# Kernel optimization log

Measured on AMD Instinct MI355X. Metric: run time of the kernel, lower is better.

The kernel has to match this reference:

```python
import jax, jax.numpy as jnp
import numpy as np

L, H, C, V, T_BLK = 12, 12, 768, 50257, 1024
D = C // H  # head dim = 64


def _layernorm(x, g, b, eps=1e-5):
    m = jnp.mean(x, axis=-1, keepdims=True)
    v = jnp.mean(jnp.square(x - m), axis=-1, keepdims=True)
    return (x - m) * jax.lax.rsqrt(v + eps) * g + b


def setup_inputs() -> dict:
    key = jax.random.key(0)
    ks = jax.random.split(key, 8)
    B, T = 8, 1024
    s = 0.02
    sp = 0.02 / np.sqrt(2 * L)  # c_proj special init
    return {
        "idx": jax.random.randint(ks[0], (B, T), 0, V, dtype=jnp.int32),
        "wte": jax.random.normal(ks[1], (V, C), jnp.float32) * s,
        "wpe": jax.random.normal(ks[2], (T_BLK, C), jnp.float32) * s,
        "ln1_g": jnp.ones((L, C), jnp.float32),
        "ln1_b": jnp.zeros((L, C), jnp.float32),
        "w_qkv": jax.random.normal(ks[3], (L, C, 3 * C), jnp.float32) * s,
        "b_qkv": jnp.zeros((L, 3 * C), jnp.float32),
        "w_ao": jax.random.normal(ks[4], (L, C, C), jnp.float32) * sp,
        "b_ao": jnp.zeros((L, C), jnp.float32),
        "ln2_g": jnp.ones((L, C), jnp.float32),
        "ln2_b": jnp.zeros((L, C), jnp.float32),
        "w_fc": jax.random.normal(ks[5], (L, C, 4 * C), jnp.float32) * s,
        "b_fc": jnp.zeros((L, 4 * C), jnp.float32),
        "w_mo": jax.random.normal(ks[6], (L, 4 * C, C), jnp.float32) * sp,
        "b_mo": jnp.zeros((L, C), jnp.float32),
        "lnf_g": jnp.ones((C,), jnp.float32),
        "lnf_b": jnp.zeros((C,), jnp.float32),
    }


def reference(idx, wte, wpe, ln1_g, ln1_b, w_qkv, b_qkv, w_ao, b_ao,
              ln2_g, ln2_b, w_fc, b_fc, w_mo, b_mo, lnf_g, lnf_b):
    B, T = idx.shape
    scale = 1.0 / np.sqrt(D)
    causal = jnp.tril(jnp.ones((T, T), dtype=bool))  # [T,T]

    x = wte[idx] + wpe[:T]  # [B,T,C]

    def block(x, p):
        g1, b1, wq, bq, wo, bo, g2, b2_, wf, bf, w2, b2m = p
        h = _layernorm(x, g1, b1)
        qkv = h @ wq + bq  # [B,T,3C]
        q, k, v = jnp.split(qkv, 3, axis=-1)
        q = q.reshape(B, T, H, D)
        k = k.reshape(B, T, H, D)
        v = v.reshape(B, T, H, D)
        att = jnp.einsum('bqhd,bkhd->bhqk', q, k) * scale
        att = jnp.where(causal, att, -jnp.inf)
        att = jax.nn.softmax(att, axis=-1)
        y = jnp.einsum('bhqk,bkhd->bqhd', att, v).reshape(B, T, C)
        x = x + y @ wo + bo
        h2 = _layernorm(x, g2, b2_)
        x = x + jax.nn.gelu(h2 @ wf + bf, approximate=False) @ w2 + b2m
        return x, None

    params = (ln1_g, ln1_b, w_qkv, b_qkv, w_ao, b_ao,
              ln2_g, ln2_b, w_fc, b_fc, w_mo, b_mo)
    x, _ = jax.lax.scan(block, x, params)

    x = _layernorm(x, lnf_g, lnf_b)
    # inference path: logits only for last position, lm_head tied to wte
    logits = x[:, -1:, :] @ wte.T  # [B,1,V]
    return logits
```

## Files before the change

### kernel.cpp

```cpp
#include <hip/hip_runtime.h>

#define B_ 8
#define T_ 1024
#define C_ 768
#define H_ 12
#define L_ 12
#define V_ 50257

typedef __bf16 bf16_t;
typedef __bf16 bf16x8 __attribute__((ext_vector_type(8)));
typedef __bf16 bf16x4 __attribute__((ext_vector_type(4)));
typedef float f32x4 __attribute__((ext_vector_type(4)));

#define AS1 __attribute__((address_space(1)))
#define AS3 __attribute__((address_space(3)))

__device__ __forceinline__ unsigned short f2bf(float f) {
  bf16_t h = (bf16_t)f;
  return __builtin_bit_cast(unsigned short, h);
}

__device__ __forceinline__ unsigned short bfbits(bf16_t h) {
  return __builtin_bit_cast(unsigned short, h);
}

__device__ __forceinline__ float fast_gelu(float v) {
  const float xe = v * 0.70710678118f;
  const float ax = fabsf(xe);
  const float t = 1.0f / fmaf(0.3275911f, ax, 1.0f);
  float poly = fmaf(t, 1.061405429f, -1.453152027f);
  poly = fmaf(t, poly, 1.421413741f);
  poly = fmaf(t, poly, -0.284496736f);
  poly = fmaf(t, poly, 0.254829592f);
  poly *= t;
  float er = 1.0f - poly * __expf(-ax * ax);
  er = (xe < 0.0f) ? -er : er;
  return 0.5f * v * (1.0f + er);
}

template<int CTRL>
__device__ __forceinline__ float dppf(float x) {
  return __builtin_bit_cast(float, __builtin_amdgcn_update_dpp(
      0, __builtin_bit_cast(int, x), CTRL, 0xF, 0xF, true));
}
__device__ __forceinline__ float red16_max(float x) {
  x = fmaxf(x, dppf<0xB1>(x));
  x = fmaxf(x, dppf<0x4E>(x));
  x = fmaxf(x, dppf<0x124>(x));
  x = fmaxf(x, dppf<0x128>(x));
  return x;
}
__device__ __forceinline__ float red16_sum(float x) {
  x += dppf<0xB1>(x);
  x += dppf<0x4E>(x);
  x += dppf<0x124>(x);
  x += dppf<0x128>(x);
  return x;
}

__global__ __launch_bounds__(192) void embed_kernel(
    const int* __restrict__ idx, const float* __restrict__ wte,
    const float* __restrict__ wpe, float* __restrict__ xf)
{
  const int bt = blockIdx.x;
  const int t = bt & (T_ - 1);
  const int tok = idx[bt];
  const int c4 = threadIdx.x << 2;
  float4 a = *(const float4*)(wte + (size_t)tok * C_ + c4);
  float4 p = *(const float4*)(wpe + (size_t)t * C_ + c4);
  float4 r; r.x = a.x + p.x; r.y = a.y + p.y; r.z = a.z + p.z; r.w = a.w + p.w;
  *(float4*)(xf + (size_t)bt * C_ + c4) = r;
}

template<bool LAST>
__global__ __launch_bounds__(256) void ln_kernel(
    const float* __restrict__ x, const float* __restrict__ gw,
    const float* __restrict__ bw, unsigned short* __restrict__ obf,
    float* __restrict__ of)
{
  __shared__ float red[8];
  const size_t row = LAST ? ((size_t)blockIdx.x * T_ + (T_ - 1)) : (size_t)blockIdx.x;
  const float* xr = x + row * C_;
  const int t = threadIdx.x;
  float v0 = xr[t], v1 = xr[t + 256], v2 = xr[t + 512];
  float s = v0 + v1 + v2;
  #pragma unroll
  for (int off = 32; off; off >>= 1) s += __shfl_xor(s, off);
  if ((t & 63) == 0) red[t >> 6] = s;
  __syncthreads();
  const float mean = (red[0] + red[1] + red[2] + red[3]) * (1.0f / C_);
  const float d0 = v0 - mean, d1 = v1 - mean, d2 = v2 - mean;
  float ss = d0 * d0 + d1 * d1 + d2 * d2;
  #pragma unroll
  for (int off = 32; off; off >>= 1) ss += __shfl_xor(ss, off);
  if ((t & 63) == 0) red[4 + (t >> 6)] = ss;
  __syncthreads();
  const float var = (red[4] + red[5] + red[6] + red[7]) * (1.0f / C_);
  const float rs = rsqrtf(var + 1e-5f);
  float o0 = d0 * rs * gw[t] + bw[t];
  float o1 = d1 * rs * gw[t + 256] + bw[t + 256];
  float o2 = d2 * rs * gw[t + 512] + bw[t + 512];
  if (LAST) {
    float* orow = of + (size_t)blockIdx.x * C_;
    orow[t] = o0; orow[t + 256] = o1; orow[t + 512] = o2;
  } else {
    unsigned short* orow = obf + row * C_;
    orow[t] = f2bf(o0); orow[t + 256] = f2bf(o1); orow[t + 512] = f2bf(o2);
  }
}

__global__ __launch_bounds__(256) void cvtw4_kernel(
    const float* __restrict__ wq, const float* __restrict__ wa,
    const float* __restrict__ wf, const float* __restrict__ wm,
    unsigned short* __restrict__ out)
{
  __shared__ float tile[32][33];
  const int i = blockIdx.x;
  const float* W; unsigned short* Wt; int K, N, tix;
  if (i < 1728)      { W = wq; Wt = out;                 K = C_;     N = 3 * C_; tix = i; }
  else if (i < 2304) { W = wa; Wt = out + 3 * C_ * C_;   K = C_;     N = C_;     tix = i - 1728; }
  else if (i < 4608) { W = wf; Wt = out + 4 * C_ * C_;   K = C_;     N = 4 * C_; tix = i - 2304; }
  else               { W = wm; Wt = out + 8 * C_ * C_;   K = 4 * C_; N = C_;     tix = i - 4608; }
  const int ntx = N >> 5;
  const int kb = (tix / ntx) << 5, nb = (tix % ntx) << 5;
  const int t = threadIdx.x;
  {
    const int k = t >> 3, n4 = (t & 7) << 2;
    float4 v = *(const float4*)(W + (size_t)(kb + k) * N + nb + n4);
    tile[k][n4] = v.x; tile[k][n4 + 1] = v.y; tile[k][n4 + 2] = v.z; tile[k][n4 + 3] = v.w;
  }
  __syncthreads();
  {
    const int n = t >> 3, k4 = (t & 7) << 2;
    ushort4 o;
    o.x = f2bf(tile[k4][n]);     o.y = f2bf(tile[k4 + 1][n]);
    o.z = f2bf(tile[k4 + 2][n]); o.w = f2bf(tile[k4 + 3][n]);
    *(ushort4*)(Wt + (size_t)(nb + n) * K + kb + k4) = o;
  }
}

template<int EPI>
__global__ __launch_bounds__(256, 2) void gemm_bt(
    const unsigned short* __restrict__ A, const unsigned short* __restrict__ Bt,
    const float* __restrict__ bias, float* __restrict__ Cf,
    unsigned short* __restrict__ Cb, int M, int N, int K, int nx)
{
  (void)M; (void)nx;
  __shared__ unsigned short As[2][128 * 64];
  __shared__ unsigned short Bs[2][128 * 64];
  const int tid = threadIdx.x;
  const int lane = tid & 63;
  const int w = tid >> 6;
  const int wr = w >> 1, wc = w & 1;
  const int l15 = lane & 15, l4 = lane >> 4;
  const int swz = lane & 7;

  const int bid = blockIdx.x;
  const int xcd = bid & 7;
  const int j = bid >> 3;
  const int mblk = xcd * 8 + (j & 7);
  const int nblk = j >> 3;
  const int m0 = mblk * 128, n0 = nblk * 128;

  f32x4 acc[4][4] = {};

  const int srow = lane >> 3;
  const int schunk = (lane & 7) ^ srow;
  const unsigned short* aSrc = A + (size_t)(m0 + w * 32 + srow) * K + schunk * 8;
  const unsigned short* bSrc = Bt + (size_t)(n0 + w * 32 + srow) * K + schunk * 8;
  const int ldsRowBase = (w * 32) * 64;

  auto stage = [&](int kt, int p) {
    const int k0 = kt << 6;
    #pragma unroll
    for (int jj = 0; jj < 4; ++jj)
      __builtin_amdgcn_global_load_lds(
          (const AS1 unsigned int*)(aSrc + (size_t)jj * 8 * K + k0),
          (AS3 unsigned int*)(&As[p][ldsRowBase + jj * 8 * 64]), 16, 0, 0);
    #pragma unroll
    for (int jj = 0; jj < 4; ++jj)
      __builtin_amdgcn_global_load_lds(
          (const AS1 unsigned int*)(bSrc + (size_t)jj * 8 * K + k0),
          (AS3 unsigned int*)(&Bs[p][ldsRowBase + jj * 8 * 64]), 16, 0, 0);
  };

  auto compute = [&](int p) {
    const unsigned short* aw = &As[p][(wr * 64) * 64];
    const unsigned short* bw2 = &Bs[p][(wc * 64) * 64];
    #pragma unroll
    for (int ks = 0; ks < 2; ++ks) {
      bf16x8 af[4], bf[4];
      #pragma unroll
      for (int mf = 0; mf < 4; ++mf)
        af[mf] = *(const bf16x8*)(aw + (mf * 16 + l15) * 64 + (((ks << 2) | l4) ^ swz) * 8);
      #pragma unroll
      for (int nf = 0; nf < 4; ++nf)
        bf[nf] = *(const bf16x8*)(bw2 + (nf * 16 + l15) * 64 + (((ks << 2) | l4) ^ swz) * 8);
      __builtin_amdgcn_s_setprio(1);
      #pragma unroll
      for (int mf = 0; mf < 4; ++mf)
        #pragma unroll
        for (int nf = 0; nf < 4; ++nf)
          acc[mf][nf] = __builtin_amdgcn_mfma_f32_16x16x32_bf16(af[mf], bf[nf], acc[mf][nf], 0, 0, 0);
      __builtin_amdgcn_s_setprio(0);
    }
  };

  const int nk = K >> 6;
  stage(0, 0);
  for (int kt = 0; kt < nk - 1; ++kt) {
    const int p = kt & 1;
    stage(kt + 1, p ^ 1);
    asm volatile("s_waitcnt vmcnt(8)" ::: "memory");
    __builtin_amdgcn_s_barrier();
    compute(p);
    __builtin_amdgcn_s_barrier();
  }
  asm volatile("s_waitcnt vmcnt(0)" ::: "memory");
  __builtin_amdgcn_s_barrier();
  compute((nk - 1) & 1);

  #pragma unroll
  for (int mf = 0; mf < 4; ++mf) {
    #pragma unroll
    for (int nf = 0; nf < 4; ++nf) {
      const int col = n0 + wc * 64 + nf * 16 + l15;
      const float bv = bias[col];
      int hh = 0, dd = 0;
      unsigned short* qkvo = nullptr;
      if constexpr (EPI == 3) {
        const int which = col / C_;
        const int rem = col - which * C_;
        hh = rem >> 6; dd = rem & 63;
        qkvo = Cb + (size_t)which * ((size_t)B_ * H_ * T_ * 64);
      }
      #pragma unroll
      for (int i = 0; i < 4; ++i) {
        const int row = m0 + wr * 64 + mf * 16 + l4 * 4 + i;
        float v = acc[mf][nf][i] + bv;
        if constexpr (EPI == 1) {
          Cf[(size_t)row * N + col] += v;
        } else if constexpr (EPI == 2) {
          Cb[(size_t)row * N + col] = f2bf(fast_gelu(v));
        } else {
          const int bb = row >> 10, tt = row & (T_ - 1);
          qkvo[(((size_t)bb * H_ + hh) * T_ + tt) * 64 + dd] = f2bf(v);
        }
      }
    }
  }
}

__global__ __launch_bounds__(256) void attn_kernel(
    const unsigned short* __restrict__ Qb, const unsigned short* __restrict__ Kb,
    const unsigned short* __restrict__ Vb, unsigned short* __restrict__ y)
{
  const int pb = blockIdx.x / 96;
  const int bh = blockIdx.x % 96;
  const int h = bh % H_;
  const int b = bh / H_;
  const int tid = threadIdx.x, lane = tid & 63, w = tid >> 6;
  const int l15 = lane & 15, l4 = lane >> 4;

  const int qband0 = pb * 64 + w * 16;
  const int qband1 = (15 - pb) * 64 + w * 16;
  const int NT = (17 - pb) >> 1;

  __shared__ unsigned short Ks[128 * 64];
  __shared__ unsigned short Vt[64 * 136];
  __shared__ unsigned short Pb[4][32 * 74];

  bf16x8 qf[2][2];
  {
    const unsigned short* q0p = Qb + ((size_t)bh * T_ + qband0) * 64;
    const unsigned short* q1p = Qb + ((size_t)bh * T_ + qband1) * 64;
    #pragma unroll
    for (int ks = 0; ks < 2; ++ks) {
      qf[0][ks] = *(const bf16x8*)(q0p + l15 * 64 + ks * 32 + l4 * 8);
      qf[1][ks] = *(const bf16x8*)(q1p + l15 * 64 + ks * 32 + l4 * 8);
    }
  }

  f32x4 o[2][4] = {};
  float mrow[2][4], lrow[2][4];
  #pragma unroll
  for (int mf = 0; mf < 2; ++mf)
    #pragma unroll
    for (int i = 0; i < 4; ++i) { mrow[mf][i] = -1e30f; lrow[mf][i] = 0.0f; }

  const unsigned short* kb0 = Kb + (size_t)bh * T_ * 64;
  const unsigned short* vb0 = Vb + (size_t)bh * T_ * 64;
  const int ck = w;
  const int skey = lane;
  const int sw = (skey & 7);

  bf16x8 kr0, kr1, kr2, kr3, vr0, vr1, vr2, vr3;
  {
    const unsigned short* kp = kb0 + (size_t)skey * 64;
    const unsigned short* vp = vb0 + (size_t)skey * 64;
    kr0 = *(const bf16x8*)(kp + ck * 8);
    kr1 = *(const bf16x8*)(kp + (ck + 4) * 8);
    kr2 = *(const bf16x8*)(kp + 64 * 64 + ck * 8);
    kr3 = *(const bf16x8*)(kp + 64 * 64 + (ck + 4) * 8);
    vr0 = *(const bf16x8*)(vp + ck * 8);
    vr1 = *(const bf16x8*)(vp + (ck + 4) * 8);
    vr2 = *(const bf16x8*)(vp + 64 * 64 + ck * 8);
    vr3 = *(const bf16x8*)(vp + 64 * 64 + (ck + 4) * 8);
  }

  for (int kt = 0; kt < NT; ++kt) {
    const int k0 = kt << 7;
    __syncthreads();
    *(bf16x8*)(Ks + skey * 64 + ((ck ^ sw) * 8)) = kr0;
    *(bf16x8*)(Ks + skey * 64 + (((ck + 4) ^ sw) * 8)) = kr1;
    *(bf16x8*)(Ks + (skey + 64) * 64 + ((ck ^ sw) * 8)) = kr2;
    *(bf16x8*)(Ks + (skey + 64) * 64 + (((ck + 4) ^ sw) * 8)) = kr3;
    #pragma unroll
    for (int jj = 0; jj < 8; ++jj) {
      Vt[(ck * 8 + jj) * 136 + skey]            = bfbits(vr0[jj]);
      Vt[((ck + 4) * 8 + jj) * 136 + skey]      = bfbits(vr1[jj]);
      Vt[(ck * 8 + jj) * 136 + skey + 64]       = bfbits(vr2[jj]);
      Vt[((ck + 4) * 8 + jj) * 136 + skey + 64] = bfbits(vr3[jj]);
    }
    __syncthreads();
    if (kt + 1 < NT) {
      const int kn = (kt + 1) << 7;
      const unsigned short* kp = kb0 + (size_t)(kn + skey) * 64;
      const unsigned short* vp = vb0 + (size_t)(kn + skey) * 64;
      kr0 = *(const bf16x8*)(kp + ck * 8);
      kr1 = *(const bf16x8*)(kp + (ck + 4) * 8);
      kr2 = *(const bf16x8*)(kp + 64 * 64 + ck * 8);
      kr3 = *(const bf16x8*)(kp + 64 * 64 + (ck + 4) * 8);
      vr0 = *(const bf16x8*)(vp + ck * 8);
      vr1 = *(const bf16x8*)(vp + (ck + 4) * 8);
      vr2 = *(const bf16x8*)(vp + 64 * 64 + ck * 8);
      vr3 = *(const bf16x8*)(vp + 64 * 64 + (ck + 4) * 8);
    }

    #pragma unroll
    for (int h2 = 0; h2 < 2; ++h2) {
      const int kh0 = k0 + h2 * 64;
      const bool act0 = (kh0 <= qband0 + 15);
      const bool act1 = (kh0 <= qband1 + 15);
      if (!act0 && !act1) continue;

      f32x4 s[2][4] = {};
      __builtin_amdgcn_s_setprio(1);
      #pragma unroll
      for (int ks = 0; ks < 2; ++ks) {
        #pragma unroll
        for (int nfk = 0; nfk < 4; ++nfk) {
          const int key = h2 * 64 + nfk * 16 + l15;
          bf16x8 kf = *(const bf16x8*)(Ks + key * 64 + ((((ks << 2) | l4) ^ (l15 & 7)) * 8));
          if (act0) s[0][nfk] = __builtin_amdgcn_mfma_f32_16x16x32_bf16(qf[0][ks], kf, s[0][nfk], 0, 0, 0);
          if (act1) s[1][nfk] = __builtin_amdgcn_mfma_f32_16x16x32_bf16(qf[1][ks], kf, s[1][nfk], 0, 0, 0);
        }
      }
      __builtin_amdgcn_s_setprio(0);

      #pragma unroll
      for (int mf = 0; mf < 2; ++mf) {
        const bool act = mf ? act1 : act0;
        if (!act) continue;
        const int qb0 = mf ? qband1 : qband0;
        const int qrow = qb0 + l4 * 4;
        const bool fullt = (kh0 + 63) <= qb0;
        float pvv[4][4], tm[4];
        #pragma unroll
        for (int i = 0; i < 4; ++i) {
          const int q = qrow + i;
          float m_ = -1e30f;
          #pragma unroll
          for (int nfk = 0; nfk < 4; ++nfk) {
            float x = s[mf][nfk][i] * 0.125f;
            x = fullt ? x : ((kh0 + nfk * 16 + l15 <= q) ? x : -1e30f);
            pvv[nfk][i] = x;
            m_ = fmaxf(m_, x);
          }
          tm[i] = red16_max(m_);
        }
        bool need = false;
        #pragma unroll
        for (int i = 0; i < 4; ++i) need |= (tm[i] > mrow[mf][i] + 8.0f);
        if (__any(need)) {
          #pragma unroll
          for (int i = 0; i < 4; ++i) {
            const float mnew = fmaxf(mrow[mf][i], tm[i]);
            const float alpha = __expf(mrow[mf][i] - mnew);
            mrow[mf][i] = mnew;
            lrow[mf][i] *= alpha;
            #pragma unroll
            for (int nf = 0; nf < 4; ++nf) o[mf][nf][i] *= alpha;
          }
        }
        #pragma unroll
        for (int i = 0; i < 4; ++i) {
          float rsum = 0.0f;
          #pragma unroll
          for (int nfk = 0; nfk < 4; ++nfk) {
            const float p = __expf(pvv[nfk][i] - mrow[mf][i]);
            pvv[nfk][i] = p; rsum += p;
          }
          rsum = red16_sum(rsum);
          lrow[mf][i] += rsum;
        }
        #pragma unroll
        for (int nfk = 0; nfk < 4; ++nfk)
          #pragma unroll
          for (int i = 0; i < 4; ++i)
            Pb[w][(mf * 16 + l4 * 4 + i) * 74 + nfk * 16 + l15] = f2bf(pvv[nfk][i]);
      }

      bf16x8 pa[2][2];
      #pragma unroll
      for (int mf = 0; mf < 2; ++mf)
        if (mf ? act1 : act0)
          #pragma unroll
          for (int k2 = 0; k2 < 2; ++k2)
            pa[mf][k2] = *(const bf16x8*)(Pb[w] + (mf * 16 + l15) * 74 + k2 * 32 + l4 * 8);
      __builtin_amdgcn_s_setprio(1);
      #pragma unroll
      for (int nf = 0; nf < 4; ++nf) {
        const int d = nf * 16 + l15;
        #pragma unroll
        for (int k2 = 0; k2 < 2; ++k2) {
          bf16x8 vf = *(const bf16x8*)(Vt + d * 136 + h2 * 64 + k2 * 32 + l4 * 8);
          if (act0) o[0][nf] = __builtin_amdgcn_mfma_f32_16x16x32_bf16(pa[0][k2], vf, o[0][nf], 0, 0, 0);
          if (act1) o[1][nf] = __builtin_amdgcn_mfma_f32_16x16x32_bf16(pa[1][k2], vf, o[1][nf], 0, 0, 0);
        }
      }
      __builtin_amdgcn_s_setprio(0);
    }
  }

  #pragma unroll
  for (int mf = 0; mf < 2; ++mf) {
    const int qb0 = mf ? qband1 : qband0;
    #pragma unroll
    for (int i = 0; i < 4; ++i) {
      const float inv = 1.0f / lrow[mf][i];
      const int q = qb0 + l4 * 4 + i;
      unsigned short* yr = y + (size_t)(b * T_ + q) * C_ + h * 64;
      #pragma unroll
      for (int nf = 0; nf < 4; ++nf)
        yr[nf * 16 + l15] = f2bf(o[mf][nf][i] * inv);
    }
  }
}

__global__ __launch_bounds__(256) void head_kernel(
    const float* __restrict__ lnf, const float* __restrict__ wte,
    float* __restrict__ out)
{
  __shared__ float xs[B_ * C_];
  for (int i = threadIdx.x; i < B_ * C_; i += 256) xs[i] = lnf[i];
  __syncthreads();
  const int w = threadIdx.x >> 6, lane = threadIdx.x & 63;
  const int v = blockIdx.x * 4 + w;
  if (v >= V_) return;
  const float* wv = wte + (size_t)v * C_ + lane * 12;
  float4 w0 = *(const float4*)(wv);
  float4 w1 = *(const float4*)(wv + 4);
  float4 w2 = *(const float4*)(wv + 8);
  float acc[B_];
  #pragma unroll
  for (int bb = 0; bb < B_; ++bb) {
    const float* xr = xs + bb * C_ + lane * 12;
    float4 x0 = *(const float4*)(xr);
    float4 x1 = *(const float4*)(xr + 4);
    float4 x2 = *(const float4*)(xr + 8);
    acc[bb] = w0.x * x0.x + w0.y * x0.y + w0.z * x0.z + w0.w * x0.w
            + w1.x * x1.x + w1.y * x1.y + w1.z * x1.z + w1.w * x1.w
            + w2.x * x2.x + w2.y * x2.y + w2.z * x2.z + w2.w * x2.w;
  }
  #pragma unroll
  for (int off = 32; off; off >>= 1) {
    #pragma unroll
    for (int bb = 0; bb < B_; ++bb)
      acc[bb] += __shfl_xor(acc[bb], off);
  }
  if (lane == 0) {
    #pragma unroll
    for (int bb = 0; bb < B_; ++bb)
      out[(size_t)bb * V_ + v] = acc[bb];
  }
}

extern "C" void kernel_launch(void* const* d_in, const int* in_sizes, int n_in,
                              void* d_out, int out_size, void* d_ws, size_t ws_size,
                              hipStream_t stream)
{
  (void)in_sizes; (void)n_in; (void)out_size; (void)ws_size;
  const int*   idx   = (const int*)d_in[0];
  const float* wte   = (const float*)d_in[1];
  const float* wpe   = (const float*)d_in[2];
  const float* ln1_g = (const float*)d_in[3];
  const float* ln1_b = (const float*)d_in[4];
  const float* w_qkv = (const float*)d_in[5];
  const float* b_qkv = (const float*)d_in[6];
  const float* w_ao  = (const float*)d_in[7];
  const float* b_ao  = (const float*)d_in[8];
  const float* ln2_g = (const float*)d_in[9];
  const float* ln2_b = (const float*)d_in[10];
  const float* w_fc  = (const float*)d_in[11];
  const float* b_fc  = (const float*)d_in[12];
  const float* w_mo  = (const float*)d_in[13];
  const float* b_mo  = (const float*)d_in[14];
  const float* lnf_g = (const float*)d_in[15];
  const float* lnf_b = (const float*)d_in[16];

  char* ws = (char*)d_ws;
  size_t off = 0;
  auto wsalloc = [&](size_t bytes) -> void* {
    void* p = ws + off;
    off += (bytes + 255) & ~(size_t)255;
    return p;
  };
  const size_t SZH = (size_t)B_ * H_ * T_ * 64;
  float* xf             = (float*)wsalloc((size_t)B_ * T_ * C_ * 4);
  unsigned short* qkv3  = (unsigned short*)wsalloc(3 * SZH * 2);
  unsigned short* a_in  = (unsigned short*)wsalloc((size_t)B_ * T_ * C_ * 2);
  unsigned short* act2  = (unsigned short*)wsalloc((size_t)B_ * T_ * 4 * C_ * 2);
  unsigned short* wbuf  = (unsigned short*)wsalloc((size_t)12 * C_ * C_ * 2);
  float* lnfb           = (float*)wsalloc((size_t)B_ * C_ * 4);

  const size_t OFF_AO = (size_t)3 * C_ * C_;
  const size_t OFF_FC = (size_t)4 * C_ * C_;
  const size_t OFF_MO = (size_t)8 * C_ * C_;
  const int MROWS = B_ * T_;

  embed_kernel<<<B_ * T_, 192, 0, stream>>>(idx, wte, wpe, xf);

  for (int l = 0; l < L_; ++l) {
    ln_kernel<false><<<B_ * T_, 256, 0, stream>>>(xf, ln1_g + l * C_, ln1_b + l * C_, a_in, nullptr);
    cvtw4_kernel<<<6912, 256, 0, stream>>>(
        w_qkv + (size_t)l * C_ * 3 * C_, w_ao + (size_t)l * C_ * C_,
        w_fc + (size_t)l * C_ * 4 * C_, w_mo + (size_t)l * 4 * C_ * C_, wbuf);
    gemm_bt<3><<<64 * 18, 256, 0, stream>>>(a_in, wbuf, b_qkv + l * 3 * C_, nullptr, qkv3, MROWS, 3 * C_, C_, 18);
    attn_kernel<<<8 * B_ * H_, 256, 0, stream>>>(qkv3, qkv3 + SZH, qkv3 + 2 * SZH, a_in);
    gemm_bt<1><<<64 * 6, 256, 0, stream>>>(a_in, wbuf + OFF_AO, b_ao + l * C_, xf, nullptr, MROWS, C_, C_, 6);
    ln_kernel<false><<<B_ * T_, 256, 0, stream>>>(xf, ln2_g + l * C_, ln2_b + l * C_, a_in, nullptr);
    gemm_bt<2><<<64 * 24, 256, 0, stream>>>(a_in, wbuf + OFF_FC, b_fc + l * 4 * C_, nullptr, act2, MROWS, 4 * C_, C_, 24);
    gemm_bt<1><<<64 * 6, 256, 0, stream>>>(act2, wbuf + OFF_MO, b_mo + l * C_, xf, nullptr, MROWS, C_, 4 * C_, 6);
  }

  ln_kernel<true><<<B_, 256, 0, stream>>>(xf, lnf_g, lnf_b, nullptr, lnfb);
  head_kernel<<<(V_ + 3) / 4, 256, 0, stream>>>(lnfb, wte, (float*)d_out);
}
```

Before: 3.659 ms.

## Batch weight conversion for all layers; single-buffer GEMM LDS for higher occupancy

Weight transpose-and-convert to bf16 now runs once for all 12 layers in a single launch before the layer loop, instead of once per layer, which removes 11 launches and makes the converted buffer 12x larger. The GEMM drops LDS double buffering: it uses one A/B tile and does a plain stage, sync, compute, sync loop, raising the launch-bounds occupancy hint from 2 to 4 blocks. This trades overlap of global-to-LDS loads with MFMA compute for more resident waves that can hide latency.

```diff
diff --git a/kernel.cpp b/kernel.cpp
--- a/kernel.cpp
+++ b/kernel.cpp
@@ -109,13 +109,19 @@
   }
 }
 
-__global__ __launch_bounds__(256) void cvtw4_kernel(
-    const float* __restrict__ wq, const float* __restrict__ wa,
-    const float* __restrict__ wf, const float* __restrict__ wm,
-    unsigned short* __restrict__ out)
+__global__ __launch_bounds__(256) void cvtwall_kernel(
+    const float* __restrict__ wq0, const float* __restrict__ wa0,
+    const float* __restrict__ wf0, const float* __restrict__ wm0,
+    unsigned short* __restrict__ out0)
 {
   __shared__ float tile[32][33];
-  const int i = blockIdx.x;
+  const int l = blockIdx.x / 6912;
+  const int i = blockIdx.x - l * 6912;
+  const float* wq = wq0 + (size_t)l * C_ * 3 * C_;
+  const float* wa = wa0 + (size_t)l * C_ * C_;
+  const float* wf = wf0 + (size_t)l * C_ * 4 * C_;
+  const float* wm = wm0 + (size_t)l * 4 * C_ * C_;
+  unsigned short* out = out0 + (size_t)l * 12 * C_ * C_;
   const float* W; unsigned short* Wt; int K, N, tix;
   if (i < 1728)      { W = wq; Wt = out;                 K = C_;     N = 3 * C_; tix = i; }
   else if (i < 2304) { W = wa; Wt = out + 3 * C_ * C_;   K = C_;     N = C_;     tix = i - 1728; }
@@ -140,14 +146,14 @@
 }
 
 template<int EPI>
-__global__ __launch_bounds__(256, 2) void gemm_bt(
+__global__ __launch_bounds__(256, 4) void gemm_bt(
     const unsigned short* __restrict__ A, const unsigned short* __restrict__ Bt,
     const float* __restrict__ bias, float* __restrict__ Cf,
     unsigned short* __restrict__ Cb, int M, int N, int K, int nx)
 {
   (void)M; (void)nx;
-  __shared__ unsigned short As[2][128 * 64];
-  __shared__ unsigned short Bs[2][128 * 64];
+  __shared__ unsigned short As[128 * 64];
+  __shared__ unsigned short Bs[128 * 64];
   const int tid = threadIdx.x;
   const int lane = tid & 63;
   const int w = tid >> 6;
@@ -170,23 +176,23 @@
   const unsigned short* bSrc = Bt + (size_t)(n0 + w * 32 + srow) * K + schunk * 8;
   const int ldsRowBase = (w * 32) * 64;
 
-  auto stage = [&](int kt, int p) {
+  auto stage = [&](int kt) {
     const int k0 = kt << 6;
     #pragma unroll
     for (int jj = 0; jj < 4; ++jj)
       __builtin_amdgcn_global_load_lds(
           (const AS1 unsigned int*)(aSrc + (size_t)jj * 8 * K + k0),
-          (AS3 unsigned int*)(&As[p][ldsRowBase + jj * 8 * 64]), 16, 0, 0);
+          (AS3 unsigned int*)(&As[ldsRowBase + jj * 8 * 64]), 16, 0, 0);
     #pragma unroll
     for (int jj = 0; jj < 4; ++jj)
       __builtin_amdgcn_global_load_lds(
           (const AS1 unsigned int*)(bSrc + (size_t)jj * 8 * K + k0),
-          (AS3 unsigned int*)(&Bs[p][ldsRowBase + jj * 8 * 64]), 16, 0, 0);
+          (AS3 unsigned int*)(&Bs[ldsRowBase + jj * 8 * 64]), 16, 0, 0);
   };
 
-  auto compute = [&](int p) {
-    const unsigned short* aw = &As[p][(wr * 64) * 64];
-    const unsigned short* bw2 = &Bs[p][(wc * 64) * 64];
+  auto compute = [&]() {
+    const unsigned short* aw = &As[(wr * 64) * 64];
+    const unsigned short* bw2 = &Bs[(wc * 64) * 64];
     #pragma unroll
     for (int ks = 0; ks < 2; ++ks) {
       bf16x8 af[4], bf[4];
@@ -207,18 +213,12 @@
   };
 
   const int nk = K >> 6;
-  stage(0, 0);
-  for (int kt = 0; kt < nk - 1; ++kt) {
-    const int p = kt & 1;
-    stage(kt + 1, p ^ 1);
-    asm volatile("s_waitcnt vmcnt(8)" ::: "memory");
-    __builtin_amdgcn_s_barrier();
-    compute(p);
-    __builtin_amdgcn_s_barrier();
-  }
-  asm volatile("s_waitcnt vmcnt(0)" ::: "memory");
-  __builtin_amdgcn_s_barrier();
-  compute((nk - 1) & 1);
+  for (int kt = 0; kt < nk; ++kt) {
+    stage(kt);
+    __syncthreads();
+    compute();
+    __syncthreads();
+  }
 
   #pragma unroll
   for (int mf = 0; mf < 4; ++mf) {
@@ -521,27 +521,27 @@
   unsigned short* qkv3  = (unsigned short*)wsalloc(3 * SZH * 2);
   unsigned short* a_in  = (unsigned short*)wsalloc((size_t)B_ * T_ * C_ * 2);
   unsigned short* act2  = (unsigned short*)wsalloc((size_t)B_ * T_ * 4 * C_ * 2);
-  unsigned short* wbuf  = (unsigned short*)wsalloc((size_t)12 * C_ * C_ * 2);
+  unsigned short* wbuf  = (unsigned short*)wsalloc((size_t)L_ * 12 * C_ * C_ * 2);
   float* lnfb           = (float*)wsalloc((size_t)B_ * C_ * 4);
 
+  const size_t WSTRIDE = (size_t)12 * C_ * C_;
   const size_t OFF_AO = (size_t)3 * C_ * C_;
   const size_t OFF_FC = (size_t)4 * C_ * C_;
   const size_t OFF_MO = (size_t)8 * C_ * C_;
   const int MROWS = B_ * T_;
 
   embed_kernel<<<B_ * T_, 192, 0, stream>>>(idx, wte, wpe, xf);
+  cvtwall_kernel<<<L_ * 6912, 256, 0, stream>>>(w_qkv, w_ao, w_fc, w_mo, wbuf);
 
   for (int l = 0; l < L_; ++l) {
+    unsigned short* wb = wbuf + (size_t)l * WSTRIDE;
     ln_kernel<false><<<B_ * T_, 256, 0, stream>>>(xf, ln1_g + l * C_, ln1_b + l * C_, a_in, nullptr);
-    cvtw4_kernel<<<6912, 256, 0, stream>>>(
-        w_qkv + (size_t)l * C_ * 3 * C_, w_ao + (size_t)l * C_ * C_,
-        w_fc + (size_t)l * C_ * 4 * C_, w_mo + (size_t)l * 4 * C_ * C_, wbuf);
-    gemm_bt<3><<<64 * 18, 256, 0, stream>>>(a_in, wbuf, b_qkv + l * 3 * C_, nullptr, qkv3, MROWS, 3 * C_, C_, 18);
+    gemm_bt<3><<<64 * 18, 256, 0, stream>>>(a_in, wb, b_qkv + l * 3 * C_, nullptr, qkv3, MROWS, 3 * C_, C_, 18);
     attn_kernel<<<8 * B_ * H_, 256, 0, stream>>>(qkv3, qkv3 + SZH, qkv3 + 2 * SZH, a_in);
-    gemm_bt<1><<<64 * 6, 256, 0, stream>>>(a_in, wbuf + OFF_AO, b_ao + l * C_, xf, nullptr, MROWS, C_, C_, 6);
+    gemm_bt<1><<<64 * 6, 256, 0, stream>>>(a_in, wb + OFF_AO, b_ao + l * C_, xf, nullptr, MROWS, C_, C_, 6);
     ln_kernel<false><<<B_ * T_, 256, 0, stream>>>(xf, ln2_g + l * C_, ln2_b + l * C_, a_in, nullptr);
-    gemm_bt<2><<<64 * 24, 256, 0, stream>>>(a_in, wbuf + OFF_FC, b_fc + l * 4 * C_, nullptr, act2, MROWS, 4 * C_, C_, 24);
-    gemm_bt<1><<<64 * 6, 256, 0, stream>>>(act2, wbuf + OFF_MO, b_mo + l * C_, xf, nullptr, MROWS, C_, 4 * C_, 6);
+    gemm_bt<2><<<64 * 24, 256, 0, stream>>>(a_in, wb + OFF_FC, b_fc + l * 4 * C_, nullptr, act2, MROWS, 4 * C_, C_, 24);
+    gemm_bt<1><<<64 * 6, 256, 0, stream>>>(act2, wb + OFF_MO, b_mo + l * C_, xf, nullptr, MROWS, C_, 4 * C_, 6);
   }
 
   ln_kernel<true><<<B_, 256, 0, stream>>>(xf, lnf_g, lnf_b, nullptr, lnfb);
```

After: 3.731 ms. Within noise of the previous version (+2.0%).
